# Performance work log

Hardware: AMD Instinct MI355X
Metric: run time of the kernel (lower is better)

The kernel has to match this reference:

```python
import jax, jax.numpy as jnp
import numpy as np
import math


def _l2norm(x, axis):
    n = jnp.sqrt(jnp.sum(x * x, axis=axis, keepdims=True))
    return x / jnp.maximum(n, 1e-12)


def _look_back(x):
    # circular shift of buckets by one along dim1, concat along window dim2
    shift = jnp.concatenate([x[:, -1:], x[:, :-1]], axis=1)
    return jnp.concatenate([shift, x], axis=2)


def _get_dup_keys(x, rounds):
    # x: [B, L, K] int; counts duplicates of each key within its row
    idx = jnp.argsort(x, axis=-1)
    s = jnp.take_along_axis(x, idx, axis=-1)
    cnt = jnp.ones(x.shape, dtype=jnp.int32)
    for i in range(1, rounds):
        eq = (s[..., i:] == s[..., :-i]).astype(jnp.int32)
        cnt = cnt.at[..., i:].add(eq)
        cnt = cnt.at[..., :-i].add(eq)
    inv = jnp.argsort(idx, axis=-1)  # unsort
    return jnp.take_along_axis(cnt, inv, axis=-1)


def _forward(query, value, rand_matrix):
    B, L, dk = query.shape
    R = rand_matrix.shape[2]
    nb = 2 * rand_matrix.shape[3]          # n_buckets
    bl = L // nb                            # bucket_length

    # ---- LSH hashing ----
    rm = rand_matrix / jnp.linalg.norm(rand_matrix, axis=1, keepdims=True)
    q_n = _l2norm(query, -1)
    mm = jnp.einsum('bld,bdrn->blrn', q_n, rm)            # [B,L,R,nb/2]
    hashes = jnp.argmax(jnp.concatenate([mm, -mm], axis=-1), axis=-1).astype(jnp.int32)
    hashes = hashes * L + jnp.arange(L, dtype=jnp.int32)[None, :, None]  # [B,L,R]

    hash_indice = jnp.argsort(hashes, axis=1)             # sort positions per round
    sorted_hashes = jnp.take_along_axis(hashes, hash_indice, axis=1)
    original_indice = jnp.argsort(hash_indice, axis=1)    # inverse permutation

    def gather_bld(x, idx):  # x [B,L,dk], idx [B,L,R] -> [B,L,dk,R]
        xe = jnp.broadcast_to(x[..., None], (B, L, dk, R))
        ie = jnp.broadcast_to(idx[:, :, None, :], (B, L, dk, R))
        return jnp.take_along_axis(xe, ie, axis=1)

    rq = gather_bld(query, hash_indice).reshape(B, nb, bl, dk, R)
    lk = _l2norm(_look_back(rq), axis=-2)                 # [B,nb,2bl,dk,R]
    mqk = jnp.einsum('bnidr,bnjdr->bnijr', rq, lk) / math.sqrt(dk)  # [B,nb,bl,2bl,R]

    # bucket mismatch mask, then causal masks (order matters: == overwrites)
    sh = (sorted_hashes // L).reshape(B, nb, bl, R)
    mqk = jnp.where(sh[:, :, :, None, :] != _look_back(sh)[:, :, None, :, :], -1e9, mqk)
    qi = hash_indice.reshape(B, nb, bl, R).astype(jnp.int32)
    ki = _look_back(qi)                                    # [B,nb,2bl,R]
    mqk = jnp.where(qi[:, :, :, None, :] < ki[:, :, None, :, :], -1e9, mqk)
    mqk = jnp.where(qi[:, :, :, None, :] == ki[:, :, None, :, :], -1e5, mqk)

    # duplicate-key counts (computed in original order, regathered to sorted order)
    ki_full = jnp.broadcast_to(ki[:, :, None, :, :], (B, nb, bl, 2 * bl, R)).reshape(B, L, 2 * bl, R)
    oi = jnp.broadcast_to(original_indice[:, :, None, :], (B, L, 2 * bl, R))
    ki_orig = jnp.take_along_axis(ki_full, oi, axis=1)
    count_key = _get_dup_keys(ki_orig.reshape(B, L, 2 * bl * R), R).reshape(B, L, 2 * bl, R)
    hi = jnp.broadcast_to(hash_indice[:, :, None, :], (B, L, 2 * bl, R))
    count_key = jnp.take_along_axis(count_key, hi, axis=1)

    mqk_flat = mqk.reshape(B, L, 2 * bl, R)
    lse = jax.scipy.special.logsumexp(mqk_flat, axis=2)   # [B,L,R]
    sm = jnp.exp(mqk_flat - jnp.log(count_key.astype(mqk.dtype)) - lse[:, :, None, :])

    rv = gather_bld(value, hash_indice).reshape(B, nb, bl, dk, R)
    att = jnp.einsum('bnijr,bnjdr->bnidr', sm.reshape(B, nb, bl, 2 * bl, R), _look_back(rv))
    att = att.reshape(B, L, dk, R)
    di = jnp.broadcast_to(original_indice[:, :, None, :], (B, L, dk, R))
    att = jnp.take_along_axis(att, di, axis=1)             # back to original order

    lse_o = jnp.take_along_axis(lse, original_indice, axis=1)
    w = jax.nn.softmax(lse_o, axis=1)                      # faithful: dim=1 as in source
    return jnp.einsum('bldr,blr->bld', att, w)


def setup_inputs() -> dict:
    key = jax.random.key(0)
    k1, k2, k3 = jax.random.split(key, 3)
    B, L, DK, R, BL = 16, 4096, 64, 4, 64
    NB = L // BL
    query = jax.random.normal(k1, (B, L, DK), dtype=jnp.float32)
    value = jax.random.normal(k2, (B, L, DK), dtype=jnp.float32)
    rand_matrix = jax.random.normal(k3, (B, DK, R, NB // 2), dtype=jnp.float32)
    return {"query": query, "value": value, "rand_matrix": rand_matrix, "seed": 0}


def reference(query, value, rand_matrix, seed):
    # eval mode: deterministic_dropout is skipped; seed unused
    return _forward(query, value, rand_matrix)
```

## Files before the change

kernel.cpp:

```cpp
#include <hip/hip_runtime.h>

#define B_ 16
#define L_ 4096
#define DK_ 64
#define R_ 4
#define NB_ 64
#define BL_ 64

typedef __attribute__((ext_vector_type(8))) short bf16x8;
typedef __attribute__((ext_vector_type(4))) float f32x4;

__device__ __forceinline__ float bf2f(unsigned short u) {
  return __uint_as_float(((unsigned)u) << 16);
}
__device__ __forceinline__ unsigned cvtpk(float lo, float hi) {
  unsigned r;
  asm("v_cvt_pk_bf16_f32 %0, %1, %2" : "=v"(r) : "v"(lo), "v"(hi));
  return r;
}
__device__ __forceinline__ int swz(int row) { return (row & 7) ^ ((row >> 3) & 7); }

__global__ __launch_bounds__(128) void prep_kernel(
    const float* __restrict__ rm, double* __restrict__ sinvd) {
  int b = blockIdx.x;
  int t = threadIdx.x;
  const float* rb = rm + (size_t)b * (DK_ * 128);
  double ss = 0.0;
  for (int d = 0; d < DK_; ++d) {
    double v = (double)rb[d * 128 + t];
    ss += v * v;
  }
  sinvd[b * 128 + t] = 1.0 / sqrt(ss);
}

__global__ __launch_bounds__(256) void hash_kernel(
    const float* __restrict__ query, const float* __restrict__ rm,
    const double* __restrict__ sinvd, int* __restrict__ bucket) {
  __shared__ float qs[64 * 68];
  __shared__ float rs[64 * 136];
  __shared__ double ssin[128];
  __shared__ int sb[64 * 4];

  int b = blockIdx.x >> 6;
  int tok0 = (blockIdx.x & 63) << 6;
  int t = threadIdx.x;

  {
    const float4* qg = (const float4*)(query + ((size_t)b * L_ + tok0) * DK_);
    #pragma unroll
    for (int u = 0; u < 4; ++u) {
      int i = t + u * 256;
      int tokl = i >> 4, c4 = i & 15;
      *(float4*)(qs + tokl * 68 + c4 * 4) = qg[i];
    }
  }
  {
    const float4* rg = (const float4*)(rm + (size_t)b * (DK_ * 128));
    #pragma unroll
    for (int u = 0; u < 8; ++u) {
      int i = t + u * 256;
      int d = i >> 5, c4 = i & 31;
      *(float4*)(rs + d * 136 + c4 * 4) = rg[i];
    }
  }
  if (t < 128) ssin[t] = sinvd[b * 128 + t];
  __syncthreads();

  int cg = t & 7;
  int tg = t >> 3;
  double acc0[16], acc1[16];
  #pragma unroll
  for (int j = 0; j < 16; ++j) { acc0[j] = 0.0; acc1[j] = 0.0; }

  const float* q0 = qs + (tg * 2 + 0) * 68;
  const float* q1 = qs + (tg * 2 + 1) * 68;
  const float* rp = rs + cg * 16;
  for (int d = 0; d < DK_; ++d) {
    double qa = (double)q0[d];
    double qb = (double)q1[d];
    const float* rr = rp + d * 136;
    #pragma unroll
    for (int j4 = 0; j4 < 4; ++j4) {
      float4 rv = *(const float4*)(rr + j4 * 4);
      double r0 = (double)rv.x, r1 = (double)rv.y,
             r2 = (double)rv.z, r3 = (double)rv.w;
      acc0[j4 * 4 + 0] += qa * r0; acc0[j4 * 4 + 1] += qa * r1;
      acc0[j4 * 4 + 2] += qa * r2; acc0[j4 * 4 + 3] += qa * r3;
      acc1[j4 * 4 + 0] += qb * r0; acc1[j4 * 4 + 1] += qb * r1;
      acc1[j4 * 4 + 2] += qb * r2; acc1[j4 * 4 + 3] += qb * r3;
    }
  }

  double bv0 = -1e300, bv1 = -1e300;
  int bi0 = 0, bi1 = 0;
  int nbase = (cg & 1) * 16;
  #pragma unroll
  for (int j = 0; j < 16; ++j) {
    int col = cg * 16 + j;
    double sv = ssin[col];
    int n = nbase + j;
    double v0 = acc0[j] * sv;
    double v1 = acc1[j] * sv;
    if (v0 > bv0 || (v0 == bv0 && n < bi0)) { bv0 = v0; bi0 = n; }
    if (-v0 > bv0 || (-v0 == bv0 && n + 32 < bi0)) { bv0 = -v0; bi0 = n + 32; }
    if (v1 > bv1 || (v1 == bv1 && n < bi1)) { bv1 = v1; bi1 = n; }
    if (-v1 > bv1 || (-v1 == bv1 && n + 32 < bi1)) { bv1 = -v1; bi1 = n + 32; }
  }
  {
    double ov = __shfl_xor(bv0, 1);
    int oi = __shfl_xor(bi0, 1);
    if (ov > bv0 || (ov == bv0 && oi < bi0)) { bv0 = ov; bi0 = oi; }
    ov = __shfl_xor(bv1, 1);
    oi = __shfl_xor(bi1, 1);
    if (ov > bv1 || (ov == bv1 && oi < bi1)) { bv1 = ov; bi1 = oi; }
  }
  if ((cg & 1) == 0) {
    int rr_ = cg >> 1;
    sb[(tg * 2 + 0) * 4 + rr_] = bi0;
    sb[(tg * 2 + 1) * 4 + rr_] = bi1;
  }
  __syncthreads();
  if (t < 64)
    ((int4*)bucket)[(size_t)b * L_ + tok0 + t] = ((int4*)sb)[t];
}

__global__ __launch_bounds__(1024) void sort_kernel(
    const int* __restrict__ bucket, int* __restrict__ sorted_pos,
    unsigned char* __restrict__ cpack) {
  int b = blockIdx.x >> 2;
  int r = blockIdx.x & 3;
  __shared__ int hist[64 * 65];
  __shared__ int off[64];
  int t = threadIdx.x, lane = t & 63, w = t >> 6;
  unsigned long long ltmask = (1ull << lane) - 1ull;
  const int* bb = bucket + (size_t)b * L_ * 4 + r;

  int binv[4], rank[4];
  #pragma unroll
  for (int u = 0; u < 4; ++u)
    binv[u] = bb[(size_t)((w * 4 + u) * 64 + lane) * 4];

  for (int idx = t; idx < 64 * 65; idx += 1024) hist[idx] = 0;
  __syncthreads();

  #pragma unroll
  for (int u = 0; u < 4; ++u) {
    int bin = binv[u];
    unsigned long long m = ~0ull;
    #pragma unroll
    for (int k = 0; k < 6; ++k) {
      unsigned long long bal = __ballot((bin >> k) & 1);
      m &= ((bin >> k) & 1) ? bal : ~bal;
    }
    rank[u] = (int)__popcll(m & ltmask);
    if (rank[u] == 0) hist[(w * 4 + u) * 65 + bin] = (int)__popcll(m);
  }
  __syncthreads();

  if (w == 0) {
    int run = 0;
    for (int g = 0; g < 64; ++g) {
      int v = hist[g * 65 + lane];
      hist[g * 65 + lane] = run;
      run += v;
    }
    int inc = run;
    #pragma unroll
    for (int d = 1; d < 64; d <<= 1) {
      int y = __shfl_up(inc, d, 64);
      if (lane >= d) inc += y;
    }
    off[lane] = inc - run;
  }
  __syncthreads();

  int* sp = sorted_pos + ((size_t)b * R_ + r) * L_;
  unsigned char* cp = cpack + (size_t)b * L_ * 4 + r;
  #pragma unroll
  for (int u = 0; u < 4; ++u) {
    int g = w * 4 + u;
    int bin = binv[u];
    int slot = off[bin] + hist[g * 65 + bin] + rank[u];
    sp[slot] = g * 64 + lane;
    cp[(size_t)(g * 64 + lane) * 4] = (unsigned char)(slot >> 6);
  }
}

__global__ __launch_bounds__(256) void attn_kernel(
    const float* __restrict__ query, const float* __restrict__ value,
    const int* __restrict__ sorted_pos, const int* __restrict__ bucket,
    const int* __restrict__ cpack,
    unsigned short* __restrict__ att, float* __restrict__ lse_s) {
  int wg = (int)blockIdx.x;
  wg = (wg & 7) * (B_ * R_ * NB_ / 8) + (wg >> 3);
  int n = wg & 63;
  int r = (wg >> 6) & 3;
  int b = wg >> 8;

  __shared__ __align__(16) short bufK[128 * 64];
  __shared__ __align__(16) unsigned short ptb[4 * 2560];
  __shared__ float ssca[64];
  __shared__ int skpos[128];
  __shared__ int sbk[128];
  __shared__ int sckp[128];

  int t = threadIdx.x;
  const int* sp = sorted_pos + ((size_t)b * R_ + r) * L_;

  if (t < 128) {
    int chunk = (t < 64) ? ((n + 63) & 63) : n;
    int pos = sp[chunk * 64 + (t & 63)];
    skpos[t] = pos;
    sbk[t] = bucket[((size_t)b * L_ + pos) * 4 + r];
    sckp[t] = ((const int*)cpack)[(size_t)b * L_ + pos];
  }
  __syncthreads();

  {
    int j = t >> 1, half = t & 1;
    const float* qr = query + ((size_t)b * L_ + skpos[j]) * DK_ + half * 32;
    float v[32];
    float ss = 0.f;
    #pragma unroll
    for (int u = 0; u < 8; ++u) {
      float4 x = ((const float4*)qr)[u];
      v[u*4+0] = x.x; v[u*4+1] = x.y; v[u*4+2] = x.z; v[u*4+3] = x.w;
      ss += x.x*x.x + x.y*x.y + x.z*x.z + x.w*x.w;
    }
    ss += __shfl_xor(ss, 1);
    float inv = 1.0f / fmaxf(sqrtf(ss), 1e-12f);
    short* krow = bufK + j * 64;
    #pragma unroll
    for (int u = 0; u < 4; ++u) {
      int d0 = half * 32 + u * 8;
      uint4 pk;
      pk.x = cvtpk(v[u*8+0] * inv, v[u*8+1] * inv);
      pk.y = cvtpk(v[u*8+2] * inv, v[u*8+3] * inv);
      pk.z = cvtpk(v[u*8+4] * inv, v[u*8+5] * inv);
      pk.w = cvtpk(v[u*8+6] * inv, v[u*8+7] * inv);
      *(uint4*)(krow + (((d0 >> 3) ^ swz(j)) << 3)) = pk;
    }
    if (j >= 64 && half == 0) ssca[j - 64] = 0.18033688f / inv;
  }
  __syncthreads();

  int l = t & 63, w = t >> 6;
  f32x4 acc[8];
  #pragma unroll
  for (int tt = 0; tt < 8; ++tt) acc[tt] = (f32x4){0.f, 0.f, 0.f, 0.f};
  {
    int qrow = 64 + w * 16 + (l & 15);
    const short* qp_ = bufK + qrow * 64;
    bf16x8 a0 = *(const bf16x8*)(qp_ + ((((l >> 4)) ^ swz(qrow)) << 3));
    bf16x8 a1 = *(const bf16x8*)(qp_ + (((4 + (l >> 4)) ^ swz(qrow)) << 3));
    #pragma unroll
    for (int tt = 0; tt < 8; ++tt) {
      int krow = tt * 16 + (l & 15);
      const short* kp_ = bufK + krow * 64;
      bf16x8 b0 = *(const bf16x8*)(kp_ + ((((l >> 4)) ^ swz(krow)) << 3));
      bf16x8 b1 = *(const bf16x8*)(kp_ + (((4 + (l >> 4)) ^ swz(krow)) << 3));
      acc[tt] = __builtin_amdgcn_mfma_f32_16x16x32_bf16(a0, b0, acc[tt], 0, 0, 0);
      acc[tt] = __builtin_amdgcn_mfma_f32_16x16x32_bf16(a1, b1, acc[tt], 0, 0, 0);
    }
  }
  __syncthreads();

  int pi = t >> 2, qd = t & 3;
  const float* vr0 = value + ((size_t)b * L_ + skpos[2 * pi]) * DK_ + qd * 16;
  const float* vr1 = value + ((size_t)b * L_ + skpos[2 * pi + 1]) * DK_ + qd * 16;
  float4 va[4], vb4[4];
  #pragma unroll
  for (int c4 = 0; c4 < 4; ++c4) { va[c4] = ((const float4*)vr0)[c4]; vb4[c4] = ((const float4*)vr1)[c4]; }

  int kp[8], bk[8], ck[8];
  #pragma unroll
  for (int tt = 0; tt < 8; ++tt) {
    int col = tt * 16 + (l & 15);
    kp[tt] = skpos[col]; bk[tt] = sbk[col]; ck[tt] = sckp[col];
  }
  float st[8][4];
  float lse[4], psum[4];
  int qprow[4];
  #pragma unroll
  for (int j = 0; j < 4; ++j) {
    int qrow = w * 16 + (l >> 4) * 4 + j;
    int qp2 = skpos[64 + qrow];
    int bq = sbk[64 + qrow];
    float csc = ssca[qrow];
    qprow[j] = qp2;
    #pragma unroll
    for (int tt = 0; tt < 8; ++tt) {
      float s = acc[tt][j] * csc;
      s = ((qp2 < kp[tt]) || (bq != bk[tt])) ? -1e9f : s;
      s = (qp2 == kp[tt]) ? -144269.5f : s;
      st[tt][j] = s;
    }
    float m = st[0][j];
    #pragma unroll
    for (int tt = 1; tt < 8; ++tt) m = fmaxf(m, st[tt][j]);
    m = fmaxf(m, __shfl_xor(m, 1));
    m = fmaxf(m, __shfl_xor(m, 2));
    m = fmaxf(m, __shfl_xor(m, 4));
    m = fmaxf(m, __shfl_xor(m, 8));
    float sum = 0.f;
    #pragma unroll
    for (int tt = 0; tt < 8; ++tt) { float e = exp2f(st[tt][j] - m); st[tt][j] = e; sum += e; }
    sum += __shfl_xor(sum, 1);
    sum += __shfl_xor(sum, 2);
    sum += __shfl_xor(sum, 4);
    sum += __shfl_xor(sum, 8);
    psum[j] = sum;
    lse[j] = 0.69314718f * (m + __log2f(sum));
  }

  #pragma unroll
  for (int j = 0; j < 4; ++j) {
    int qrow = w * 16 + (l >> 4) * 4 + j;
    unsigned aq = (unsigned)sckp[64 + qrow] | 0x40404040u;
    float isum = 1.0f / psum[j];
    #pragma unroll
    for (int tt = 0; tt < 8; ++tt) {
      unsigned e = (aq - (unsigned)ck[tt]) & 0x3E3E3E3Eu;
      unsigned y = (e - 0x01010101u) & ~e & 0x80808080u;
      float cntf = (float)__popc(y);
      st[tt][j] = st[tt][j] * isum * __builtin_amdgcn_rcpf(cntf);
    }
  }
  if ((l & 15) == 0) {
    #pragma unroll
    for (int j = 0; j < 4; ++j)
      lse_s[((size_t)b * R_ + r) * L_ + qprow[j]] = lse[j];
  }

  {
    unsigned short* PT = ptb + w * 2560;
    int q0 = (l >> 4) * 4;
    #pragma unroll
    for (int tt = 0; tt < 8; ++tt) {
      unsigned u0 = cvtpk(st[tt][0], st[tt][1]);
      unsigned u1 = cvtpk(st[tt][2], st[tt][3]);
      int krow = tt * 16 + (l & 15);
      *(uint2*)(PT + krow * 20 + q0) = make_uint2(u0, u1);
    }
  }

  short* VT = bufK;
  #pragma unroll
  for (int c4 = 0; c4 < 4; ++c4) {
    float4 x0 = va[c4], x1 = vb4[c4];
    #pragma unroll
    for (int cc = 0; cc < 4; ++cc) {
      float f0 = (cc == 0) ? x0.x : (cc == 1) ? x0.y : (cc == 2) ? x0.z : x0.w;
      float f1 = (cc == 0) ? x1.x : (cc == 1) ? x1.y : (cc == 2) ? x1.z : x1.w;
      unsigned pk2 = cvtpk(f0, f1);
      int nrow = qd * 16 + c4 * 4 + cc;
      int k0 = 2 * pi;
      int a = nrow * 128 + (((k0 >> 3) ^ swz(nrow)) << 3) + (k0 & 7);
      *(unsigned*)(VT + a) = pk2;
    }
  }
  __syncthreads();

  f32x4 o[4];
  #pragma unroll
  for (int nt = 0; nt < 4; ++nt) o[nt] = (f32x4){0.f, 0.f, 0.f, 0.f};
  {
    const unsigned short* PTr = ptb + w * 2560;
    #pragma unroll
    for (int ks = 0; ks < 4; ++ks) {
      int basePT = (ks * 32 + (l >> 4) * 8) * 20 + (l & 15);
      union { uint4 u; bf16x8 v; } bp;
      bp.u.x = (unsigned)PTr[basePT]       | ((unsigned)PTr[basePT + 20] << 16);
      bp.u.y = (unsigned)PTr[basePT + 40]  | ((unsigned)PTr[basePT + 60] << 16);
      bp.u.z = (unsigned)PTr[basePT + 80]  | ((unsigned)PTr[basePT + 100] << 16);
      bp.u.w = (unsigned)PTr[basePT + 120] | ((unsigned)PTr[basePT + 140] << 16);
      #pragma unroll
      for (int nt = 0; nt < 4; ++nt) {
        int vrow = nt * 16 + (l & 15);
        bf16x8 av = *(const bf16x8*)(VT + vrow * 128 + (((ks * 4 + (l >> 4)) ^ swz(vrow)) << 3));
        o[nt] = __builtin_amdgcn_mfma_f32_16x16x32_bf16(av, bp.v, o[nt], 0, 0, 0);
      }
    }
  }

  {
    int qpos = skpos[64 + w * 16 + (l & 15)];
    unsigned short* arow = att + (((size_t)b * R_ + r) * L_ + qpos) * DK_;
    #pragma unroll
    for (int nt = 0; nt < 4; ++nt) {
      unsigned p0 = cvtpk(o[nt][0], o[nt][1]);
      unsigned p1 = cvtpk(o[nt][2], o[nt][3]);
      *(uint2*)(arow + nt * 16 + (l >> 4) * 4) = make_uint2(p0, p1);
    }
  }
}

__global__ __launch_bounds__(256) void lsered_kernel(
    const float* __restrict__ lse_s, float* __restrict__ wred) {
  int br = blockIdx.x;
  const float* row = lse_s + (size_t)br * L_;
  __shared__ float red[4];
  int t = threadIdx.x;
  float m = -1e30f;
  for (int p = t; p < L_; p += 256) m = fmaxf(m, row[p]);
  #pragma unroll
  for (int mask = 1; mask < 64; mask <<= 1) m = fmaxf(m, __shfl_xor(m, mask, 64));
  if ((t & 63) == 0) red[t >> 6] = m;
  __syncthreads();
  m = fmaxf(fmaxf(red[0], red[1]), fmaxf(red[2], red[3]));
  __syncthreads();
  float sum = 0.f;
  for (int p = t; p < L_; p += 256) sum += __expf(row[p] - m);
  #pragma unroll
  for (int mask = 1; mask < 64; mask <<= 1) sum += __shfl_xor(sum, mask, 64);
  if ((t & 63) == 0) red[t >> 6] = sum;
  __syncthreads();
  if (t == 0) {
    wred[br * 2] = m;
    wred[br * 2 + 1] = red[0] + red[1] + red[2] + red[3];
  }
}

__global__ __launch_bounds__(256) void combine_kernel(
    const unsigned short* __restrict__ att, const float* __restrict__ lse_s,
    const float* __restrict__ wred, float* __restrict__ out) {
  int idx = blockIdx.x * 256 + threadIdx.x;
  int dq = idx & 3;
  int l = (idx >> 2) & (L_ - 1);
  int b = idx >> 14;
  float wv[4];
  #pragma unroll
  for (int r = 0; r < R_; ++r) {
    float m = wred[(b * R_ + r) * 2];
    float sinv = 1.0f / wred[(b * R_ + r) * 2 + 1];
    wv[r] = __expf(lse_s[((size_t)b * R_ + r) * L_ + l] - m) * sinv;
  }
  #pragma unroll
  for (int u = 0; u < 4; ++u) {
    int d4 = dq * 4 + u;
    float4 o = make_float4(0.f, 0.f, 0.f, 0.f);
    #pragma unroll
    for (int r = 0; r < R_; ++r) {
      ushort4 a = *(const ushort4*)(att + ((((size_t)b * R_ + r) * L_ + l) * 16 + d4) * 4);
      o.x += wv[r] * bf2f(a.x); o.y += wv[r] * bf2f(a.y);
      o.z += wv[r] * bf2f(a.z); o.w += wv[r] * bf2f(a.w);
    }
    ((float4*)out)[((size_t)b * L_ + l) * 16 + d4] = o;
  }
}

extern "C" void kernel_launch(void* const* d_in, const int* in_sizes, int n_in,
                              void* d_out, int out_size, void* d_ws, size_t ws_size,
                              hipStream_t stream) {
  const float* query = (const float*)d_in[0];
  const float* value = (const float*)d_in[1];
  const float* rm    = (const float*)d_in[2];
  (void)in_sizes; (void)n_in; (void)out_size; (void)ws_size;

  char* ws = (char*)d_ws;
  const size_t ATT_BYTES = (size_t)B_ * R_ * L_ * DK_ * 2;
  const size_t MB = 1048576;
  unsigned short* att        = (unsigned short*)ws;
  int*            bucket     = (int*)(ws + ATT_BYTES);
  int*            sorted_pos = (int*)(ws + ATT_BYTES + 1 * MB);
  unsigned char*  cpack      = (unsigned char*)(ws + ATT_BYTES + 2 * MB);
  float*          lse_s      = (float*)(ws + ATT_BYTES + 3 * MB);
  float*          wred       = (float*)(ws + ATT_BYTES + 4 * MB);
  double*         sinvd      = (double*)(ws + ATT_BYTES + 5 * MB);
  float* out = (float*)d_out;

  prep_kernel<<<B_, 128, 0, stream>>>(rm, sinvd);
  hash_kernel<<<B_ * 64, 256, 0, stream>>>(query, rm, sinvd, bucket);
  sort_kernel<<<B_ * R_, 1024, 0, stream>>>(bucket, sorted_pos, cpack);
  attn_kernel<<<B_ * R_ * NB_, 256, 0, stream>>>(query, value, sorted_pos, bucket,
                                                 (const int*)cpack, att, lse_s);
  lsered_kernel<<<B_ * R_, 256, 0, stream>>>(lse_s, wred);
  combine_kernel<<<(B_ * L_ * 4) / 256, 256, 0, stream>>>(att, lse_s, wred, out);
}
```

Before: 122.8 us.

## Transpose QK MFMA to keep probabilities in registers and drop LDS P staging

```diff
diff --git a/kernel.cpp b/kernel.cpp
--- a/kernel.cpp
+++ b/kernel.cpp
@@ -198,11 +198,10 @@
   int b = wg >> 8;
 
   __shared__ __align__(16) short bufK[128 * 64];
-  __shared__ __align__(16) unsigned short ptb[4 * 2560];
   __shared__ float ssca[64];
   __shared__ int skpos[128];
-  __shared__ int sbk[128];
-  __shared__ int sckp[128];
+  __shared__ int skcode[128];
+  __shared__ int sck[128];
 
   int t = threadIdx.x;
   const int* sp = sorted_pos + ((size_t)b * R_ + r) * L_;
@@ -210,9 +209,10 @@
   if (t < 128) {
     int chunk = (t < 64) ? ((n + 63) & 63) : n;
     int pos = sp[chunk * 64 + (t & 63)];
+    int bkt = bucket[((size_t)b * L_ + pos) * 4 + r];
     skpos[t] = pos;
-    sbk[t] = bucket[((size_t)b * L_ + pos) * 4 + r];
-    sckp[t] = ((const int*)cpack)[(size_t)b * L_ + pos];
+    skcode[t] = (bkt << 12) | pos;
+    sck[t] = ((const int*)cpack)[(size_t)b * L_ + pos];
   }
   __syncthreads();
 
@@ -245,22 +245,23 @@
   __syncthreads();
 
   int l = t & 63, w = t >> 6;
+  int g = l >> 4, c = l & 15;
   f32x4 acc[8];
   #pragma unroll
   for (int tt = 0; tt < 8; ++tt) acc[tt] = (f32x4){0.f, 0.f, 0.f, 0.f};
   {
-    int qrow = 64 + w * 16 + (l & 15);
+    int qrow = 64 + w * 16 + c;
     const short* qp_ = bufK + qrow * 64;
-    bf16x8 a0 = *(const bf16x8*)(qp_ + ((((l >> 4)) ^ swz(qrow)) << 3));
-    bf16x8 a1 = *(const bf16x8*)(qp_ + (((4 + (l >> 4)) ^ swz(qrow)) << 3));
+    bf16x8 q0 = *(const bf16x8*)(qp_ + (((g) ^ swz(qrow)) << 3));
+    bf16x8 q1 = *(const bf16x8*)(qp_ + (((4 + g) ^ swz(qrow)) << 3));
     #pragma unroll
     for (int tt = 0; tt < 8; ++tt) {
-      int krow = tt * 16 + (l & 15);
+      int krow = tt * 16 + c;
       const short* kp_ = bufK + krow * 64;
-      bf16x8 b0 = *(const bf16x8*)(kp_ + ((((l >> 4)) ^ swz(krow)) << 3));
-      bf16x8 b1 = *(const bf16x8*)(kp_ + (((4 + (l >> 4)) ^ swz(krow)) << 3));
-      acc[tt] = __builtin_amdgcn_mfma_f32_16x16x32_bf16(a0, b0, acc[tt], 0, 0, 0);
-      acc[tt] = __builtin_amdgcn_mfma_f32_16x16x32_bf16(a1, b1, acc[tt], 0, 0, 0);
+      bf16x8 k0 = *(const bf16x8*)(kp_ + (((g) ^ swz(krow)) << 3));
+      bf16x8 k1 = *(const bf16x8*)(kp_ + (((4 + g) ^ swz(krow)) << 3));
+      acc[tt] = __builtin_amdgcn_mfma_f32_16x16x32_bf16(k0, q0, acc[tt], 0, 0, 0);
+      acc[tt] = __builtin_amdgcn_mfma_f32_16x16x32_bf16(k1, q1, acc[tt], 0, 0, 0);
     }
   }
   __syncthreads();
@@ -272,76 +273,63 @@
   #pragma unroll
   for (int c4 = 0; c4 < 4; ++c4) { va[c4] = ((const float4*)vr0)[c4]; vb4[c4] = ((const float4*)vr1)[c4]; }
 
-  int kp[8], bk[8], ck[8];
+  int qi = w * 16 + c;
+  int qcode = skcode[64 + qi];
+  unsigned aq = (unsigned)sck[64 + qi] | 0x40404040u;
+  float csc = ssca[qi];
+  int qpos = qcode & 4095;
+
+  float m = -1e30f;
   #pragma unroll
   for (int tt = 0; tt < 8; ++tt) {
-    int col = tt * 16 + (l & 15);
-    kp[tt] = skpos[col]; bk[tt] = sbk[col]; ck[tt] = sckp[col];
-  }
-  float st[8][4];
-  float lse[4], psum[4];
-  int qprow[4];
-  #pragma unroll
-  for (int j = 0; j < 4; ++j) {
-    int qrow = w * 16 + (l >> 4) * 4 + j;
-    int qp2 = skpos[64 + qrow];
-    int bq = sbk[64 + qrow];
-    float csc = ssca[qrow];
-    qprow[j] = qp2;
-    #pragma unroll
-    for (int tt = 0; tt < 8; ++tt) {
+    int4 kc = *(const int4*)(skcode + tt * 16 + g * 4);
+    #pragma unroll
+    for (int j = 0; j < 4; ++j) {
+      int kcode = (j == 0) ? kc.x : (j == 1) ? kc.y : (j == 2) ? kc.z : kc.w;
       float s = acc[tt][j] * csc;
-      s = ((qp2 < kp[tt]) || (bq != bk[tt])) ? -1e9f : s;
-      s = (qp2 == kp[tt]) ? -144269.5f : s;
-      st[tt][j] = s;
-    }
-    float m = st[0][j];
-    #pragma unroll
-    for (int tt = 1; tt < 8; ++tt) m = fmaxf(m, st[tt][j]);
-    m = fmaxf(m, __shfl_xor(m, 1));
-    m = fmaxf(m, __shfl_xor(m, 2));
-    m = fmaxf(m, __shfl_xor(m, 4));
-    m = fmaxf(m, __shfl_xor(m, 8));
-    float sum = 0.f;
-    #pragma unroll
-    for (int tt = 0; tt < 8; ++tt) { float e = exp2f(st[tt][j] - m); st[tt][j] = e; sum += e; }
-    sum += __shfl_xor(sum, 1);
-    sum += __shfl_xor(sum, 2);
-    sum += __shfl_xor(sum, 4);
-    sum += __shfl_xor(sum, 8);
-    psum[j] = sum;
-    lse[j] = 0.69314718f * (m + __log2f(sum));
-  }
-
-  #pragma unroll
-  for (int j = 0; j < 4; ++j) {
-    int qrow = w * 16 + (l >> 4) * 4 + j;
-    unsigned aq = (unsigned)sckp[64 + qrow] | 0x40404040u;
-    float isum = 1.0f / psum[j];
-    #pragma unroll
-    for (int tt = 0; tt < 8; ++tt) {
-      unsigned e = (aq - (unsigned)ck[tt]) & 0x3E3E3E3Eu;
+      unsigned x = (unsigned)(qcode ^ kcode);
+      s = ((qcode < kcode) || (x >= 4096u)) ? -1e9f : s;
+      s = (x == 0u) ? -144269.5f : s;
+      acc[tt][j] = s;
+      m = fmaxf(m, s);
+    }
+  }
+  m = fmaxf(m, __shfl_xor(m, 16));
+  m = fmaxf(m, __shfl_xor(m, 32));
+  float sum = 0.f;
+  #pragma unroll
+  for (int tt = 0; tt < 8; ++tt) {
+    #pragma unroll
+    for (int j = 0; j < 4; ++j) {
+      float e = exp2f(acc[tt][j] - m);
+      acc[tt][j] = e;
+      sum += e;
+    }
+  }
+  sum += __shfl_xor(sum, 16);
+  sum += __shfl_xor(sum, 32);
+  float lse = 0.69314718f * (m + __log2f(sum));
+  float isum = 1.0f / sum;
+  if (l < 16) lse_s[((size_t)b * R_ + r) * L_ + qpos] = lse;
+
+  #pragma unroll
+  for (int tt = 0; tt < 8; ++tt) {
+    int4 c4v = *(const int4*)(sck + tt * 16 + g * 4);
+    #pragma unroll
+    for (int j = 0; j < 4; ++j) {
+      int ckv = (j == 0) ? c4v.x : (j == 1) ? c4v.y : (j == 2) ? c4v.z : c4v.w;
+      unsigned e = (aq - (unsigned)ckv) & 0x3E3E3E3Eu;
       unsigned y = (e - 0x01010101u) & ~e & 0x80808080u;
       float cntf = (float)__popc(y);
-      st[tt][j] = st[tt][j] * isum * __builtin_amdgcn_rcpf(cntf);
-    }
-  }
-  if ((l & 15) == 0) {
-    #pragma unroll
-    for (int j = 0; j < 4; ++j)
-      lse_s[((size_t)b * R_ + r) * L_ + qprow[j]] = lse[j];
-  }
-
-  {
-    unsigned short* PT = ptb + w * 2560;
-    int q0 = (l >> 4) * 4;
-    #pragma unroll
-    for (int tt = 0; tt < 8; ++tt) {
-      unsigned u0 = cvtpk(st[tt][0], st[tt][1]);
-      unsigned u1 = cvtpk(st[tt][2], st[tt][3]);
-      int krow = tt * 16 + (l & 15);
-      *(uint2*)(PT + krow * 20 + q0) = make_uint2(u0, u1);
-    }
+      acc[tt][j] = acc[tt][j] * isum * __builtin_amdgcn_rcpf(cntf);
+    }
+  }
+
+  unsigned pk01[8], pk23[8];
+  #pragma unroll
+  for (int tt = 0; tt < 8; ++tt) {
+    pk01[tt] = cvtpk(acc[tt][0], acc[tt][1]);
+    pk23[tt] = cvtpk(acc[tt][2], acc[tt][3]);
   }
 
   short* VT = bufK;
@@ -365,32 +353,36 @@
   #pragma unroll
   for (int nt = 0; nt < 4; ++nt) o[nt] = (f32x4){0.f, 0.f, 0.f, 0.f};
   {
-    const unsigned short* PTr = ptb + w * 2560;
+    int src  = (g & 1) * 32 + c;
+    int srcB = src + 16;
+    bool sel = (l >= 32);
     #pragma unroll
     for (int ks = 0; ks < 4; ++ks) {
-      int basePT = (ks * 32 + (l >> 4) * 8) * 20 + (l & 15);
+      unsigned xA = __shfl(pk01[2 * ks], src),  yA = __shfl(pk01[2 * ks + 1], src);
+      unsigned xB = __shfl(pk23[2 * ks], src),  yB = __shfl(pk23[2 * ks + 1], src);
+      unsigned xC = __shfl(pk01[2 * ks], srcB), yC = __shfl(pk01[2 * ks + 1], srcB);
+      unsigned xD = __shfl(pk23[2 * ks], srcB), yD = __shfl(pk23[2 * ks + 1], srcB);
       union { uint4 u; bf16x8 v; } bp;
-      bp.u.x = (unsigned)PTr[basePT]       | ((unsigned)PTr[basePT + 20] << 16);
-      bp.u.y = (unsigned)PTr[basePT + 40]  | ((unsigned)PTr[basePT + 60] << 16);
-      bp.u.z = (unsigned)PTr[basePT + 80]  | ((unsigned)PTr[basePT + 100] << 16);
-      bp.u.w = (unsigned)PTr[basePT + 120] | ((unsigned)PTr[basePT + 140] << 16);
+      bp.u.x = sel ? yA : xA;
+      bp.u.y = sel ? yB : xB;
+      bp.u.z = sel ? yC : xC;
+      bp.u.w = sel ? yD : xD;
       #pragma unroll
       for (int nt = 0; nt < 4; ++nt) {
-        int vrow = nt * 16 + (l & 15);
-        bf16x8 av = *(const bf16x8*)(VT + vrow * 128 + (((ks * 4 + (l >> 4)) ^ swz(vrow)) << 3));
+        int vrow = nt * 16 + c;
+        bf16x8 av = *(const bf16x8*)(VT + vrow * 128 + (((ks * 4 + g) ^ swz(vrow)) << 3));
         o[nt] = __builtin_amdgcn_mfma_f32_16x16x32_bf16(av, bp.v, o[nt], 0, 0, 0);
       }
     }
   }
 
   {
-    int qpos = skpos[64 + w * 16 + (l & 15)];
     unsigned short* arow = att + (((size_t)b * R_ + r) * L_ + qpos) * DK_;
     #pragma unroll
     for (int nt = 0; nt < 4; ++nt) {
       unsigned p0 = cvtpk(o[nt][0], o[nt][1]);
       unsigned p1 = cvtpk(o[nt][2], o[nt][3]);
-      *(uint2*)(arow + nt * 16 + (l >> 4) * 4) = make_uint2(p0, p1);
+      *(uint2*)(arow + nt * 16 + g * 4) = make_uint2(p0, p1);
     }
   }
 }
```

After: 120.8 us. Within noise of the previous version (-1.6%).
